# Optimization experiments

Measured on AMD Instinct MI355X. Metric: run time of the kernel, lower is better.

Reference implementation:

```python
import jax, jax.numpy as jnp
import numpy as np

HEAD_NUM = 8
NEG_BIG = 1.0e9


def setup_inputs() -> dict:
    key = jax.random.key(0)
    ks = jax.random.split(key, 9)
    B, S, D = 8, 1024, 512
    return {
        "query": jax.random.normal(ks[0], (B, S, D), dtype=jnp.float32),
        "key": jax.random.normal(ks[1], (B, S, D), dtype=jnp.float32),
        "value": jax.random.normal(ks[2], (B, S, D), dtype=jnp.float32),
        "query_mask": jax.random.randint(ks[3], (B, S), 0, 2, dtype=jnp.int32),
        "key_mask": jax.random.randint(ks[4], (B, S), 0, 2, dtype=jnp.int32),
        "Wq": jax.random.normal(ks[5], (D, D), dtype=jnp.float32) * (1.0 / np.sqrt(D)),
        "Wk": jax.random.normal(ks[6], (D, D), dtype=jnp.float32) * (1.0 / np.sqrt(D)),
        "Wv": jax.random.normal(ks[7], (D, D), dtype=jnp.float32) * (1.0 / np.sqrt(D)),
        "Wo": jax.random.normal(ks[8], (D, D), dtype=jnp.float32) * (1.0 / np.sqrt(D)),
    }


def _split_heads(x, h):
    # TF: tf.concat(tf.split(x, h, axis=2), axis=0) -> (h*B, S, D//h), head-major rows
    return jnp.concatenate(jnp.split(x, h, axis=2), axis=0)


def reference(query, key, value, query_mask, key_mask, Wq, Wk, Wv, Wo):
    H = HEAD_NUM
    B, Sq, Dq = query.shape
    Sk = key.shape[1]
    D = value.shape[-1]

    q = query @ Wq   # (B, Sq, D)
    k = key @ Wk     # (B, Sk, D)
    v = value @ Wv   # (B, Sk, D)

    q_ = _split_heads(q, H)  # (H*B, Sq, D/H)
    k_ = _split_heads(k, H)
    v_ = _split_heads(v, H)

    # TF _reshape_mask: tile then reshape -> batch-major (b*H + h) rows (faithful)
    km = jnp.reshape(jnp.tile(key_mask[:, None, :], (1, H, 1)), (-1, Sk))

    sims = jnp.einsum('bqd,bkd->bqk', q_, k_) / jnp.sqrt(jnp.float32(Dq))

    # causal band mask (sequence_mask=True)
    ones = jnp.ones((Sq, Sk), dtype=jnp.float32)
    causal = ones - jnp.tril(ones)
    sims = sims - causal[None, :, :] * NEG_BIG

    # additive key padding mask
    sims = sims - (1.0 - km[:, None, :].astype(jnp.float32)) * NEG_BIG

    att = jax.nn.softmax(sims, axis=-1)            # (H*B, Sq, Sk)
    out = jnp.einsum('bqk,bkd->bqd', att, v_)      # (H*B, Sq, D/H)

    # faithful TF recombination: reshape (-1, H, Sq, D/H) -> transpose -> (-1, Sq, D)
    out = out.reshape(-1, H, Sq, D // H).transpose(0, 2, 1, 3).reshape(-1, Sq, D)

    out = out @ Wo
    out = jax.nn.relu(out)
    out = out * query_mask[:, :, None].astype(jnp.float32)
    return out
```

## Files before the change

### kernel.cpp

```cpp
#include <hip/hip_runtime.h>
#include <hip/hip_bf16.h>

typedef __bf16 bf16_t;
typedef __bf16 bf16x8 __attribute__((ext_vector_type(8)));
typedef float f32x4 __attribute__((ext_vector_type(4)));

static __device__ __forceinline__ f32x4 mfma16x16x32(bf16x8 a, bf16x8 b, f32x4 c) {
    return __builtin_amdgcn_mfma_f32_16x16x32_bf16(a, b, c, 0, 0, 0);
}

__global__ __launch_bounds__(256, 2) void gemm_qkv(
        const float* __restrict__ Aq, const float* __restrict__ Ak, const float* __restrict__ Av,
        const float* __restrict__ Wq, const float* __restrict__ Wk, const float* __restrict__ Wv,
        bf16_t* __restrict__ Oq, bf16_t* __restrict__ Ok, bf16_t* __restrict__ Ov) {
    __shared__ bf16_t As[128][40];
    __shared__ bf16_t Bs[128][40];

    const int tid  = threadIdx.x;
    const int lane = tid & 63;
    const int wave = tid >> 6;
    const int l15  = lane & 15;
    const int kgrp = lane >> 4;
    const int wr   = wave >> 1;
    const int wc   = wave & 1;

    const int row0 = blockIdx.x * 128;
    const int col0 = blockIdx.y * 128;
    const int z    = blockIdx.z;

    const float* A = (z == 0) ? Aq : (z == 1) ? Ak : Av;
    const float* W = (z == 0) ? Wq : (z == 1) ? Wk : Wv;

    const int ar  = tid >> 1;
    const int ach = (tid & 1) * 16;
    const int bc  = tid & 127;
    const int bkh = (tid >> 7) * 16;

    f32x4 acc[4][4];
    #pragma unroll
    for (int m = 0; m < 4; ++m)
        #pragma unroll
        for (int n = 0; n < 4; ++n) acc[m][n] = (f32x4){0.f, 0.f, 0.f, 0.f};

    float4 areg[4];
    float  breg[16];
    const float* Abase = A + (size_t)(row0 + ar) * 512 + ach;
    const float* Wbase = W + (size_t)bkh * 512 + col0 + bc;

    #pragma unroll
    for (int i = 0; i < 4; ++i) areg[i] = *(const float4*)(Abase + i * 4);
    #pragma unroll
    for (int i = 0; i < 16; ++i) breg[i] = Wbase[(size_t)i * 512];

    for (int kb0 = 0; kb0 < 512; kb0 += 32) {
        __syncthreads();
        {
            bf16x8 w0, w1;
            #pragma unroll
            for (int i = 0; i < 4; ++i) { w0[i] = (bf16_t)(&areg[0].x)[i]; w0[i + 4] = (bf16_t)(&areg[1].x)[i]; }
            #pragma unroll
            for (int i = 0; i < 4; ++i) { w1[i] = (bf16_t)(&areg[2].x)[i]; w1[i + 4] = (bf16_t)(&areg[3].x)[i]; }
            *(bf16x8*)&As[ar][ach]     = w0;
            *(bf16x8*)&As[ar][ach + 8] = w1;
            bf16x8 b0, b1;
            #pragma unroll
            for (int i = 0; i < 8; ++i) { b0[i] = (bf16_t)breg[i]; b1[i] = (bf16_t)breg[i + 8]; }
            *(bf16x8*)&Bs[bc][bkh]     = b0;
            *(bf16x8*)&Bs[bc][bkh + 8] = b1;
        }
        __syncthreads();
        if (kb0 + 32 < 512) {
            const float* An = Abase + kb0 + 32;
            #pragma unroll
            for (int i = 0; i < 4; ++i) areg[i] = *(const float4*)(An + i * 4);
            const float* Wn = Wbase + (size_t)(kb0 + 32) * 512;
            #pragma unroll
            for (int i = 0; i < 16; ++i) breg[i] = Wn[(size_t)i * 512];
        }
        bf16x8 af[4], bf[4];
        #pragma unroll
        for (int m = 0; m < 4; ++m) af[m] = *(const bf16x8*)&As[wr * 64 + m * 16 + l15][kgrp * 8];
        #pragma unroll
        for (int n = 0; n < 4; ++n) bf[n] = *(const bf16x8*)&Bs[wc * 64 + n * 16 + l15][kgrp * 8];
        __builtin_amdgcn_s_setprio(1);
        #pragma unroll
        for (int m = 0; m < 4; ++m)
            #pragma unroll
            for (int n = 0; n < 4; ++n)
                acc[m][n] = mfma16x16x32(af[m], bf[n], acc[m][n]);
        __builtin_amdgcn_s_setprio(0);
    }

    bf16_t* O = (z == 0) ? Oq : (z == 1) ? Ok : Ov;
    #pragma unroll
    for (int m = 0; m < 4; ++m)
        #pragma unroll
        for (int j = 0; j < 4; ++j) {
            const int r = row0 + wr * 64 + m * 16 + kgrp * 4 + j;
            #pragma unroll
            for (int n = 0; n < 4; ++n) {
                const int c = col0 + wc * 64 + n * 16 + l15;
                if (z < 2) {
                    O[(size_t)r * 512 + c] = (bf16_t)acc[m][n][j];
                } else {
                    const int bb = r >> 10, ss = r & 1023;
                    O[((size_t)bb * 512 + c) * 1024 + ss] = (bf16_t)acc[m][n][j];
                }
            }
        }
}

__global__ __launch_bounds__(256, 2) void gemm_out(const bf16_t* __restrict__ Ab,
                                                   const float* __restrict__ W,
                                                   float* __restrict__ Out,
                                                   const int* __restrict__ qmask) {
    __shared__ bf16_t As[128][40];
    __shared__ bf16_t Bs[128][40];

    const int tid  = threadIdx.x;
    const int lane = tid & 63;
    const int wave = tid >> 6;
    const int l15  = lane & 15;
    const int kgrp = lane >> 4;
    const int wr   = wave >> 1;
    const int wc   = wave & 1;

    const int row0 = blockIdx.x * 128;
    const int col0 = blockIdx.y * 128;

    const int ar  = tid >> 1;
    const int ach = (tid & 1) * 16;
    const int bc  = tid & 127;
    const int bkh = (tid >> 7) * 16;

    f32x4 acc[4][4];
    #pragma unroll
    for (int m = 0; m < 4; ++m)
        #pragma unroll
        for (int n = 0; n < 4; ++n) acc[m][n] = (f32x4){0.f, 0.f, 0.f, 0.f};

    bf16x8 areg[2];
    float  breg[16];
    const bf16_t* Abase = Ab + (size_t)(row0 + ar) * 512 + ach;
    const float*  Wbase = W + (size_t)bkh * 512 + col0 + bc;

    areg[0] = *(const bf16x8*)Abase;
    areg[1] = *(const bf16x8*)(Abase + 8);
    #pragma unroll
    for (int i = 0; i < 16; ++i) breg[i] = Wbase[(size_t)i * 512];

    for (int kb0 = 0; kb0 < 512; kb0 += 32) {
        __syncthreads();
        *(bf16x8*)&As[ar][ach]     = areg[0];
        *(bf16x8*)&As[ar][ach + 8] = areg[1];
        {
            bf16x8 b0, b1;
            #pragma unroll
            for (int i = 0; i < 8; ++i) { b0[i] = (bf16_t)breg[i]; b1[i] = (bf16_t)breg[i + 8]; }
            *(bf16x8*)&Bs[bc][bkh]     = b0;
            *(bf16x8*)&Bs[bc][bkh + 8] = b1;
        }
        __syncthreads();
        if (kb0 + 32 < 512) {
            const bf16_t* An = Abase + kb0 + 32;
            areg[0] = *(const bf16x8*)An;
            areg[1] = *(const bf16x8*)(An + 8);
            const float* Wn = Wbase + (size_t)(kb0 + 32) * 512;
            #pragma unroll
            for (int i = 0; i < 16; ++i) breg[i] = Wn[(size_t)i * 512];
        }
        bf16x8 af[4], bf[4];
        #pragma unroll
        for (int m = 0; m < 4; ++m) af[m] = *(const bf16x8*)&As[wr * 64 + m * 16 + l15][kgrp * 8];
        #pragma unroll
        for (int n = 0; n < 4; ++n) bf[n] = *(const bf16x8*)&Bs[wc * 64 + n * 16 + l15][kgrp * 8];
        __builtin_amdgcn_s_setprio(1);
        #pragma unroll
        for (int m = 0; m < 4; ++m)
            #pragma unroll
            for (int n = 0; n < 4; ++n)
                acc[m][n] = mfma16x16x32(af[m], bf[n], acc[m][n]);
        __builtin_amdgcn_s_setprio(0);
    }

    #pragma unroll
    for (int m = 0; m < 4; ++m)
        #pragma unroll
        for (int j = 0; j < 4; ++j) {
            const int r = row0 + wr * 64 + m * 16 + kgrp * 4 + j;
            const float fq = (float)qmask[r];
            #pragma unroll
            for (int n = 0; n < 4; ++n) {
                const int c = col0 + wc * 64 + n * 16 + l15;
                Out[(size_t)r * 512 + c] = fmaxf(acc[m][n][j], 0.0f) * fq;
            }
        }
}

__global__ __launch_bounds__(256, 3) void attn_flash(const bf16_t* __restrict__ qb,
                                                     const bf16_t* __restrict__ kb,
                                                     const bf16_t* __restrict__ vtb,
                                                     const int* __restrict__ key_mask,
                                                     bf16_t* __restrict__ attout) {
    __shared__ char shbuf[34816];
    bf16_t (*P)[32][68] = (bf16_t(*)[32][68])shbuf;
    float (*Omg)[32][66] = (float(*)[32][66])shbuf;
    float* mmg = (float*)(shbuf + 33792);
    float* lmg = (float*)(shbuf + 33792 + 512);

    const int tid  = threadIdx.x;
    const int lane = tid & 63;
    const int w    = tid >> 6;
    const int l15  = lane & 15;
    const int kgrp = lane >> 4;

    const int hb = blockIdx.x;
    const int h  = hb >> 3;
    const int b  = hb & 7;
    const int qw = (31 - (int)blockIdx.y) * 32;

    const size_t bS512 = (size_t)b * 1024 * 512;
    const int hoff = h * 64;
    const int* km = key_mask + h * 1024;

    int kmv = km[lane];
    unsigned long long bal = __ballot(kmv != 0);
    int first1 = bal ? (__ffsll(bal) - 1) : 64;
    const int ntiles = (qw < first1) ? 16 : ((qw + 95) >> 6);

    bf16x8 aq[2][2];
    #pragma unroll
    for (int rf = 0; rf < 2; ++rf)
        #pragma unroll
        for (int ks = 0; ks < 2; ++ks)
            aq[rf][ks] = *(const bf16x8*)(qb + bS512 + (size_t)(qw + rf * 16 + l15) * 512
                                          + hoff + ks * 32 + kgrp * 8);

    f32x4 O[2][4];
    float m[2][4], l[2][4];
    #pragma unroll
    for (int rf = 0; rf < 2; ++rf) {
        #pragma unroll
        for (int df = 0; df < 4; ++df) O[rf][df] = (f32x4){0.f, 0.f, 0.f, 0.f};
        #pragma unroll
        for (int j = 0; j < 4; ++j) { m[rf][j] = -3.0e38f; l[rf][j] = 0.f; }
    }

    const float scale = 0.044194173824159216f;
    const bf16_t* kbase = kb + bS512 + hoff;
    const bf16_t* vbase = vtb + ((size_t)b * 512 + hoff) * 1024;

    for (int kt = w; kt < ntiles; kt += 4) {
        const int kt0 = kt * 64;

        f32x4 S[2][4];
        #pragma unroll
        for (int rf = 0; rf < 2; ++rf)
            #pragma unroll
            for (int cf = 0; cf < 4; ++cf) S[rf][cf] = (f32x4){0.f, 0.f, 0.f, 0.f};

        __builtin_amdgcn_s_setprio(1);
        #pragma unroll
        for (int cf = 0; cf < 4; ++cf) {
            const bf16_t* krow = kbase + (size_t)(kt0 + cf * 16 + l15) * 512 + kgrp * 8;
            bf16x8 bk0 = *(const bf16x8*)krow;
            bf16x8 bk1 = *(const bf16x8*)(krow + 32);
            S[0][cf] = mfma16x16x32(aq[0][0], bk0, S[0][cf]);
            S[0][cf] = mfma16x16x32(aq[0][1], bk1, S[0][cf]);
            S[1][cf] = mfma16x16x32(aq[1][0], bk0, S[1][cf]);
            S[1][cf] = mfma16x16x32(aq[1][1], bk1, S[1][cf]);
        }
        __builtin_amdgcn_s_setprio(0);

        float kmadd[4];
        #pragma unroll
        for (int cf = 0; cf < 4; ++cf)
            kmadd[cf] = (km[kt0 + cf * 16 + l15] == 0) ? 1.0e9f : 0.0f;

        float mx[2][4];
        #pragma unroll
        for (int rf = 0; rf < 2; ++rf)
            #pragma unroll
            for (int j = 0; j < 4; ++j) {
                const int qrow = qw + rf * 16 + kgrp * 4 + j;
                float mj = -3.0e38f;
                #pragma unroll
                for (int cf = 0; cf < 4; ++cf) {
                    float s = S[rf][cf][j] * scale;
                    if (kt0 + cf * 16 + l15 > qrow) s -= 1.0e9f;
                    s -= kmadd[cf];
                    S[rf][cf][j] = s;
                    mj = fmaxf(mj, s);
                }
                mx[rf][j] = mj;
            }
        #pragma unroll
        for (int off = 1; off < 16; off <<= 1)
            #pragma unroll
            for (int rf = 0; rf < 2; ++rf)
                #pragma unroll
                for (int j = 0; j < 4; ++j)
                    mx[rf][j] = fmaxf(mx[rf][j], __shfl_xor(mx[rf][j], off));

        float fac[2][4];
        #pragma unroll
        for (int rf = 0; rf < 2; ++rf)
            #pragma unroll
            for (int j = 0; j < 4; ++j) {
                float mn = fmaxf(m[rf][j], mx[rf][j]);
                fac[rf][j] = __expf(m[rf][j] - mn);
                m[rf][j] = mn;
            }
        #pragma unroll
        for (int rf = 0; rf < 2; ++rf)
            #pragma unroll
            for (int j = 0; j < 4; ++j) {
                float ps = 0.f;
                #pragma unroll
                for (int cf = 0; cf < 4; ++cf) {
                    float p = __expf(S[rf][cf][j] - m[rf][j]);
                    S[rf][cf][j] = p;
                    ps += p;
                }
                l[rf][j] = l[rf][j] * fac[rf][j] + ps;
            }
        #pragma unroll
        for (int rf = 0; rf < 2; ++rf)
            #pragma unroll
            for (int df = 0; df < 4; ++df)
                #pragma unroll
                for (int j = 0; j < 4; ++j)
                    O[rf][df][j] *= fac[rf][j];

        #pragma unroll
        for (int rf = 0; rf < 2; ++rf)
            #pragma unroll
            for (int cf = 0; cf < 4; ++cf)
                #pragma unroll
                for (int j = 0; j < 4; ++j)
                    P[w][rf * 16 + kgrp * 4 + j][cf * 16 + l15] = (bf16_t)S[rf][cf][j];
        asm volatile("s_waitcnt lgkmcnt(0)" ::: "memory");

        bf16x8 pa[2][2];
        #pragma unroll
        for (int rf = 0; rf < 2; ++rf)
            #pragma unroll
            for (int ks = 0; ks < 2; ++ks)
                pa[rf][ks] = *(const bf16x8*)&P[w][rf * 16 + l15][ks * 32 + kgrp * 8];

        __builtin_amdgcn_s_setprio(1);
        #pragma unroll
        for (int df = 0; df < 4; ++df) {
            const bf16_t* vrow = vbase + (size_t)(df * 16 + l15) * 1024 + kt0 + kgrp * 8;
            bf16x8 vf0 = *(const bf16x8*)vrow;
            bf16x8 vf1 = *(const bf16x8*)(vrow + 32);
            O[0][df] = mfma16x16x32(pa[0][0], vf0, O[0][df]);
            O[0][df] = mfma16x16x32(pa[0][1], vf1, O[0][df]);
            O[1][df] = mfma16x16x32(pa[1][0], vf0, O[1][df]);
            O[1][df] = mfma16x16x32(pa[1][1], vf1, O[1][df]);
        }
        __builtin_amdgcn_s_setprio(0);
    }

    __syncthreads();

    #pragma unroll
    for (int rf = 0; rf < 2; ++rf)
        #pragma unroll
        for (int j = 0; j < 4; ++j) {
            float lv = l[rf][j];
            #pragma unroll
            for (int off = 1; off < 16; off <<= 1) lv += __shfl_xor(lv, off);
            l[rf][j] = lv;
        }

    #pragma unroll
    for (int rf = 0; rf < 2; ++rf)
        #pragma unroll
        for (int df = 0; df < 4; ++df)
            #pragma unroll
            for (int j = 0; j < 4; ++j)
                Omg[w][rf * 16 + kgrp * 4 + j][df * 16 + l15] = O[rf][df][j];
    if (l15 == 0) {
        #pragma unroll
        for (int rf = 0; rf < 2; ++rf)
            #pragma unroll
            for (int j = 0; j < 4; ++j) {
                mmg[w * 32 + rf * 16 + kgrp * 4 + j] = m[rf][j];
                lmg[w * 32 + rf * 16 + kgrp * 4 + j] = l[rf][j];
            }
    }
    __syncthreads();

    {
        const int r  = tid >> 3;
        const int c0 = (tid & 7) * 8;
        float m0 = mmg[r], m1 = mmg[32 + r], m2 = mmg[64 + r], m3 = mmg[96 + r];
        float M = fmaxf(fmaxf(m0, m1), fmaxf(m2, m3));
        float f0 = __expf(m0 - M), f1 = __expf(m1 - M);
        float f2 = __expf(m2 - M), f3 = __expf(m3 - M);
        float ls = lmg[r] * f0 + lmg[32 + r] * f1 + lmg[64 + r] * f2 + lmg[96 + r] * f3;
        float inv = 1.0f / ls;
        bf16_t outv[8];
        #pragma unroll
        for (int i = 0; i < 8; ++i) {
            float acc = Omg[0][r][c0 + i] * f0 + Omg[1][r][c0 + i] * f1
                      + Omg[2][r][c0 + i] * f2 + Omg[3][r][c0 + i] * f3;
            outv[i] = (bf16_t)(acc * inv);
        }
        *(bf16x8*)&attout[(size_t)(h * 1024 + qw + r) * 512 + b * 64 + c0] = *(bf16x8*)outv;
    }
}

extern "C" void kernel_launch(void* const* d_in, const int* in_sizes, int n_in,
                              void* d_out, int out_size, void* d_ws, size_t ws_size,
                              hipStream_t stream) {
    const float* query = (const float*)d_in[0];
    const float* key   = (const float*)d_in[1];
    const float* value = (const float*)d_in[2];
    const int*   qmask = (const int*)d_in[3];
    const int*   kmask = (const int*)d_in[4];
    const float* Wq    = (const float*)d_in[5];
    const float* Wk    = (const float*)d_in[6];
    const float* Wv    = (const float*)d_in[7];
    const float* Wo    = (const float*)d_in[8];
    float* out = (float*)d_out;

    const size_t NELEM = (size_t)8 * 1024 * 512;
    bf16_t* qb  = (bf16_t*)d_ws;
    bf16_t* kb  = qb + NELEM;
    bf16_t* vtb = kb + NELEM;
    bf16_t* ab  = vtb + NELEM;

    gemm_qkv<<<dim3(64, 4, 3), dim3(256), 0, stream>>>(query, key, value, Wq, Wk, Wv, qb, kb, vtb);
    attn_flash<<<dim3(64, 32), dim3(256), 0, stream>>>(qb, kb, vtb, kmask, ab);
    gemm_out<<<dim3(64, 4), dim3(256), 0, stream>>>(ab, Wo, out, qmask);
}
```

Measured before the change: 110.0 us.

## Pair mirrored causal query chunks per block and fold softmax scale into Q

Each attention block now handles two query chunks, y and 31-y, so causal work per block is balanced. This halves the grid, and tiles from the two chunks are interleaved in proportion. The softmax scale and log2(e) are folded into the Q projection epilogue, so the kernel can use exp2 directly and skip the per-score multiply. The causal comparison is also skipped for tiles wholly below the diagonal. In exchange, register pressure doubles from two sets of accumulators and Q fragments, which may lower occupancy, and there is a second merge phase with extra barriers.

```diff
diff --git a/kernel.cpp b/kernel.cpp
--- a/kernel.cpp
+++ b/kernel.cpp
@@ -4,6 +4,9 @@
 typedef __bf16 bf16_t;
 typedef __bf16 bf16x8 __attribute__((ext_vector_type(8)));
 typedef float f32x4 __attribute__((ext_vector_type(4)));
+
+#define CPOW 1.4426950409e9f
+#define QSCALE 0.063758715f
 
 static __device__ __forceinline__ f32x4 mfma16x16x32(bf16x8 a, bf16x8 b, f32x4 c) {
     return __builtin_amdgcn_mfma_f32_16x16x32_bf16(a, b, c, 0, 0, 0);
@@ -92,6 +95,7 @@
     }
 
     bf16_t* O = (z == 0) ? Oq : (z == 1) ? Ok : Ov;
+    const float esc = (z == 0) ? QSCALE : 1.0f;
     #pragma unroll
     for (int m = 0; m < 4; ++m)
         #pragma unroll
@@ -101,7 +105,7 @@
             for (int n = 0; n < 4; ++n) {
                 const int c = col0 + wc * 64 + n * 16 + l15;
                 if (z < 2) {
-                    O[(size_t)r * 512 + c] = (bf16_t)acc[m][n][j];
+                    O[(size_t)r * 512 + c] = (bf16_t)(acc[m][n][j] * esc);
                 } else {
                     const int bb = r >> 10, ss = r & 1023;
                     O[((size_t)bb * 512 + c) * 1024 + ss] = (bf16_t)acc[m][n][j];
@@ -217,7 +221,9 @@
     const int hb = blockIdx.x;
     const int h  = hb >> 3;
     const int b  = hb & 7;
-    const int qw = (31 - (int)blockIdx.y) * 32;
+    const int y  = blockIdx.y;
+    const int qwA = y * 32;
+    const int qwB = (31 - y) * 32;
 
     const size_t bS512 = (size_t)b * 1024 * 512;
     const int hoff = h * 64;
@@ -226,31 +232,37 @@
     int kmv = km[lane];
     unsigned long long bal = __ballot(kmv != 0);
     int first1 = bal ? (__ffsll(bal) - 1) : 64;
-    const int ntiles = (qw < first1) ? 16 : ((qw + 95) >> 6);
-
-    bf16x8 aq[2][2];
+    const int ntA = (qwA < first1) ? 16 : ((qwA + 95) >> 6);
+    const int ntB = (qwB < first1) ? 16 : ((qwB + 95) >> 6);
+    const int na  = (ntA > w) ? ((ntA - w + 3) >> 2) : 0;
+    const int nb  = (ntB > w) ? ((ntB - w + 3) >> 2) : 0;
+
+    bf16x8 aqA[2][2], aqB[2][2];
     #pragma unroll
     for (int rf = 0; rf < 2; ++rf)
         #pragma unroll
-        for (int ks = 0; ks < 2; ++ks)
-            aq[rf][ks] = *(const bf16x8*)(qb + bS512 + (size_t)(qw + rf * 16 + l15) * 512
-                                          + hoff + ks * 32 + kgrp * 8);
-
-    f32x4 O[2][4];
-    float m[2][4], l[2][4];
+        for (int ks = 0; ks < 2; ++ks) {
+            aqA[rf][ks] = *(const bf16x8*)(qb + bS512 + (size_t)(qwA + rf * 16 + l15) * 512
+                                           + hoff + ks * 32 + kgrp * 8);
+            aqB[rf][ks] = *(const bf16x8*)(qb + bS512 + (size_t)(qwB + rf * 16 + l15) * 512
+                                           + hoff + ks * 32 + kgrp * 8);
+        }
+
+    f32x4 OA[2][4], OB[2][4];
+    float mA[2][4], lA[2][4], mB[2][4], lB[2][4];
     #pragma unroll
     for (int rf = 0; rf < 2; ++rf) {
         #pragma unroll
-        for (int df = 0; df < 4; ++df) O[rf][df] = (f32x4){0.f, 0.f, 0.f, 0.f};
-        #pragma unroll
-        for (int j = 0; j < 4; ++j) { m[rf][j] = -3.0e38f; l[rf][j] = 0.f; }
+        for (int df = 0; df < 4; ++df) { OA[rf][df] = (f32x4){0.f,0.f,0.f,0.f}; OB[rf][df] = (f32x4){0.f,0.f,0.f,0.f}; }
+        #pragma unroll
+        for (int j = 0; j < 4; ++j) { mA[rf][j] = -3.0e38f; lA[rf][j] = 0.f; mB[rf][j] = -3.0e38f; lB[rf][j] = 0.f; }
     }
 
-    const float scale = 0.044194173824159216f;
     const bf16_t* kbase = kb + bS512 + hoff;
     const bf16_t* vbase = vtb + ((size_t)b * 512 + hoff) * 1024;
 
-    for (int kt = w; kt < ntiles; kt += 4) {
+    auto processTile = [&](int kt, int qwX, bf16x8 (&aq)[2][2], f32x4 (&O)[2][4],
+                           float (&m)[2][4], float (&l)[2][4], int pslot) {
         const int kt0 = kt * 64;
 
         f32x4 S[2][4];
@@ -275,20 +287,21 @@
         float kmadd[4];
         #pragma unroll
         for (int cf = 0; cf < 4; ++cf)
-            kmadd[cf] = (km[kt0 + cf * 16 + l15] == 0) ? 1.0e9f : 0.0f;
-
+            kmadd[cf] = (km[kt0 + cf * 16 + l15] == 0) ? CPOW : 0.0f;
+
+        const bool needC = (kt0 + 63 > qwX);
         float mx[2][4];
         #pragma unroll
         for (int rf = 0; rf < 2; ++rf)
             #pragma unroll
             for (int j = 0; j < 4; ++j) {
-                const int qrow = qw + rf * 16 + kgrp * 4 + j;
+                const int qrow = qwX + rf * 16 + kgrp * 4 + j;
                 float mj = -3.0e38f;
                 #pragma unroll
                 for (int cf = 0; cf < 4; ++cf) {
-                    float s = S[rf][cf][j] * scale;
-                    if (kt0 + cf * 16 + l15 > qrow) s -= 1.0e9f;
-                    s -= kmadd[cf];
+                    float sub = kmadd[cf];
+                    if (needC && (kt0 + cf * 16 + l15 > qrow)) sub += CPOW;
+                    float s = S[rf][cf][j] - sub;
                     S[rf][cf][j] = s;
                     mj = fmaxf(mj, s);
                 }
@@ -308,7 +321,7 @@
             #pragma unroll
             for (int j = 0; j < 4; ++j) {
                 float mn = fmaxf(m[rf][j], mx[rf][j]);
-                fac[rf][j] = __expf(m[rf][j] - mn);
+                fac[rf][j] = __builtin_amdgcn_exp2f(m[rf][j] - mn);
                 m[rf][j] = mn;
             }
         #pragma unroll
@@ -318,7 +331,7 @@
                 float ps = 0.f;
                 #pragma unroll
                 for (int cf = 0; cf < 4; ++cf) {
-                    float p = __expf(S[rf][cf][j] - m[rf][j]);
+                    float p = __builtin_amdgcn_exp2f(S[rf][cf][j] - m[rf][j]);
                     S[rf][cf][j] = p;
                     ps += p;
                 }
@@ -338,7 +351,7 @@
             for (int cf = 0; cf < 4; ++cf)
                 #pragma unroll
                 for (int j = 0; j < 4; ++j)
-                    P[w][rf * 16 + kgrp * 4 + j][cf * 16 + l15] = (bf16_t)S[rf][cf][j];
+                    P[pslot][rf * 16 + kgrp * 4 + j][cf * 16 + l15] = (bf16_t)S[rf][cf][j];
         asm volatile("s_waitcnt lgkmcnt(0)" ::: "memory");
 
         bf16x8 pa[2][2];
@@ -346,7 +359,7 @@
         for (int rf = 0; rf < 2; ++rf)
             #pragma unroll
             for (int ks = 0; ks < 2; ++ks)
-                pa[rf][ks] = *(const bf16x8*)&P[w][rf * 16 + l15][ks * 32 + kgrp * 8];
+                pa[rf][ks] = *(const bf16x8*)&P[pslot][rf * 16 + l15][ks * 32 + kgrp * 8];
 
         __builtin_amdgcn_s_setprio(1);
         #pragma unroll
@@ -360,56 +373,72 @@
             O[1][df] = mfma16x16x32(pa[1][1], vf1, O[1][df]);
         }
         __builtin_amdgcn_s_setprio(0);
+    };
+
+    {
+        int ia = 0, ib = 0;
+        const int total = na + nb;
+        for (int it = 0; it < total; ++it) {
+            bool doA;
+            if (ia >= na) doA = false;
+            else if (ib >= nb) doA = true;
+            else doA = (ia * nb <= ib * na);
+            if (doA) { processTile(w + 4 * ia, qwA, aqA, OA, mA, lA, w);     ++ia; }
+            else     { processTile(w + 4 * ib, qwB, aqB, OB, mB, lB, 4 + w); ++ib; }
+        }
     }
 
+    auto mergeChunk = [&](int qwX, f32x4 (&O)[2][4], float (&m)[2][4], float (&l)[2][4]) {
+        #pragma unroll
+        for (int rf = 0; rf < 2; ++rf)
+            #pragma unroll
+            for (int j = 0; j < 4; ++j) {
+                float lv = l[rf][j];
+                #pragma unroll
+                for (int off = 1; off < 16; off <<= 1) lv += __shfl_xor(lv, off);
+                l[rf][j] = lv;
+            }
+        #pragma unroll
+        for (int rf = 0; rf < 2; ++rf)
+            #pragma unroll
+            for (int df = 0; df < 4; ++df)
+                #pragma unroll
+                for (int j = 0; j < 4; ++j)
+                    Omg[w][rf * 16 + kgrp * 4 + j][df * 16 + l15] = O[rf][df][j];
+        if (l15 == 0) {
+            #pragma unroll
+            for (int rf = 0; rf < 2; ++rf)
+                #pragma unroll
+                for (int j = 0; j < 4; ++j) {
+                    mmg[w * 32 + rf * 16 + kgrp * 4 + j] = m[rf][j];
+                    lmg[w * 32 + rf * 16 + kgrp * 4 + j] = l[rf][j];
+                }
+        }
+        __syncthreads();
+        {
+            const int r  = tid >> 3;
+            const int c0 = (tid & 7) * 8;
+            float m0 = mmg[r], m1 = mmg[32 + r], m2 = mmg[64 + r], m3 = mmg[96 + r];
+            float M = fmaxf(fmaxf(m0, m1), fmaxf(m2, m3));
+            float f0 = __builtin_amdgcn_exp2f(m0 - M), f1 = __builtin_amdgcn_exp2f(m1 - M);
+            float f2 = __builtin_amdgcn_exp2f(m2 - M), f3 = __builtin_amdgcn_exp2f(m3 - M);
+            float ls = lmg[r] * f0 + lmg[32 + r] * f1 + lmg[64 + r] * f2 + lmg[96 + r] * f3;
+            float inv = 1.0f / ls;
+            bf16_t outv[8];
+            #pragma unroll
+            for (int i = 0; i < 8; ++i) {
+                float acc = Omg[0][r][c0 + i] * f0 + Omg[1][r][c0 + i] * f1
+                          + Omg[2][r][c0 + i] * f2 + Omg[3][r][c0 + i] * f3;
+                outv[i] = (bf16_t)(acc * inv);
+            }
+            *(bf16x8*)&attout[(size_t)(h * 1024 + qwX + r) * 512 + b * 64 + c0] = *(bf16x8*)outv;
+        }
+    };
+
     __syncthreads();
-
-    #pragma unroll
-    for (int rf = 0; rf < 2; ++rf)
-        #pragma unroll
-        for (int j = 0; j < 4; ++j) {
-            float lv = l[rf][j];
-            #pragma unroll
-            for (int off = 1; off < 16; off <<= 1) lv += __shfl_xor(lv, off);
-            l[rf][j] = lv;
-        }
-
-    #pragma unroll
-    for (int rf = 0; rf < 2; ++rf)
-        #pragma unroll
-        for (int df = 0; df < 4; ++df)
-            #pragma unroll
-            for (int j = 0; j < 4; ++j)
-                Omg[w][rf * 16 + kgrp * 4 + j][df * 16 + l15] = O[rf][df][j];
-    if (l15 == 0) {
-        #pragma unroll
-        for (int rf = 0; rf < 2; ++rf)
-            #pragma unroll
-            for (int j = 0; j < 4; ++j) {
-                mmg[w * 32 + rf * 16 + kgrp * 4 + j] = m[rf][j];
-                lmg[w * 32 + rf * 16 + kgrp * 4 + j] = l[rf][j];
-            }
-    }
+    mergeChunk(qwA, OA, mA, lA);
     __syncthreads();
-
-    {
-        const int r  = tid >> 3;
-        const int c0 = (tid & 7) * 8;
-        float m0 = mmg[r], m1 = mmg[32 + r], m2 = mmg[64 + r], m3 = mmg[96 + r];
-        float M = fmaxf(fmaxf(m0, m1), fmaxf(m2, m3));
-        float f0 = __expf(m0 - M), f1 = __expf(m1 - M);
-        float f2 = __expf(m2 - M), f3 = __expf(m3 - M);
-        float ls = lmg[r] * f0 + lmg[32 + r] * f1 + lmg[64 + r] * f2 + lmg[96 + r] * f3;
-        float inv = 1.0f / ls;
-        bf16_t outv[8];
-        #pragma unroll
-        for (int i = 0; i < 8; ++i) {
-            float acc = Omg[0][r][c0 + i] * f0 + Omg[1][r][c0 + i] * f1
-                      + Omg[2][r][c0 + i] * f2 + Omg[3][r][c0 + i] * f3;
-            outv[i] = (bf16_t)(acc * inv);
-        }
-        *(bf16x8*)&attout[(size_t)(h * 1024 + qw + r) * 512 + b * 64 + c0] = *(bf16x8*)outv;
-    }
+    mergeChunk(qwB, OB, mB, lB);
 }
 
 extern "C" void kernel_launch(void* const* d_in, const int* in_sizes, int n_in,
@@ -433,6 +462,6 @@
     bf16_t* ab  = vtb + NELEM;
 
     gemm_qkv<<<dim3(64, 4, 3), dim3(256), 0, stream>>>(query, key, value, Wq, Wk, Wv, qb, kb, vtb);
-    attn_flash<<<dim3(64, 32), dim3(256), 0, stream>>>(qb, kb, vtb, kmask, ab);
+    attn_flash<<<dim3(64, 16), dim3(256), 0, stream>>>(qb, kb, vtb, kmask, ab);
     gemm_out<<<dim3(64, 4), dim3(256), 0, stream>>>(ab, Wo, out, qmask);
 }
```

After: 170.8 us. +55.2%, slower.

## Fold softmax scale and log2e into Q projection, use exp2, shrink attention LDS

Applied to the files above, without the earlier changes.

Pre-scales Q in the projection GEMM epilogue by scale*log2(e), so the attention kernel can drop the per-element multiply and use the hardware exp2 instruction with mask constants scaled to match. The causal-mask comparison is skipped for key tiles entirely below the diagonal. The cross-wave merge buffer is stored in bf16 instead of fp32, which shrinks shared memory so the launch bound can be raised from 3 to 6 blocks per CU. In exchange, the partial outputs lose precision before they are merged, and register pressure is tighter at the higher occupancy target.

```diff
diff --git a/kernel.cpp b/kernel.cpp
--- a/kernel.cpp
+++ b/kernel.cpp
@@ -4,6 +4,9 @@
 typedef __bf16 bf16_t;
 typedef __bf16 bf16x8 __attribute__((ext_vector_type(8)));
 typedef float f32x4 __attribute__((ext_vector_type(4)));
+
+#define CPOW 1.4426950409e9f
+#define QSCALE 0.063758715f
 
 static __device__ __forceinline__ f32x4 mfma16x16x32(bf16x8 a, bf16x8 b, f32x4 c) {
     return __builtin_amdgcn_mfma_f32_16x16x32_bf16(a, b, c, 0, 0, 0);
@@ -92,6 +95,7 @@
     }
 
     bf16_t* O = (z == 0) ? Oq : (z == 1) ? Ok : Ov;
+    const float esc = (z == 0) ? QSCALE : 1.0f;
     #pragma unroll
     for (int m = 0; m < 4; ++m)
         #pragma unroll
@@ -101,7 +105,7 @@
             for (int n = 0; n < 4; ++n) {
                 const int c = col0 + wc * 64 + n * 16 + l15;
                 if (z < 2) {
-                    O[(size_t)r * 512 + c] = (bf16_t)acc[m][n][j];
+                    O[(size_t)r * 512 + c] = (bf16_t)(acc[m][n][j] * esc);
                 } else {
                     const int bb = r >> 10, ss = r & 1023;
                     O[((size_t)bb * 512 + c) * 1024 + ss] = (bf16_t)acc[m][n][j];
@@ -197,16 +201,16 @@
         }
 }
 
-__global__ __launch_bounds__(256, 3) void attn_flash(const bf16_t* __restrict__ qb,
+__global__ __launch_bounds__(256, 6) void attn_flash(const bf16_t* __restrict__ qb,
                                                      const bf16_t* __restrict__ kb,
                                                      const bf16_t* __restrict__ vtb,
                                                      const int* __restrict__ key_mask,
                                                      bf16_t* __restrict__ attout) {
-    __shared__ char shbuf[34816];
-    bf16_t (*P)[32][68] = (bf16_t(*)[32][68])shbuf;
-    float (*Omg)[32][66] = (float(*)[32][66])shbuf;
-    float* mmg = (float*)(shbuf + 33792);
-    float* lmg = (float*)(shbuf + 33792 + 512);
+    __shared__ char shbuf[19456];
+    bf16_t (*P)[32][72]   = (bf16_t(*)[32][72])shbuf;
+    bf16_t (*Omg)[32][72] = (bf16_t(*)[32][72])shbuf;
+    float* mmg = (float*)(shbuf + 18432);
+    float* lmg = (float*)(shbuf + 18432 + 512);
 
     const int tid  = threadIdx.x;
     const int lane = tid & 63;
@@ -246,7 +250,6 @@
         for (int j = 0; j < 4; ++j) { m[rf][j] = -3.0e38f; l[rf][j] = 0.f; }
     }
 
-    const float scale = 0.044194173824159216f;
     const bf16_t* kbase = kb + bS512 + hoff;
     const bf16_t* vbase = vtb + ((size_t)b * 512 + hoff) * 1024;
 
@@ -275,8 +278,9 @@
         float kmadd[4];
         #pragma unroll
         for (int cf = 0; cf < 4; ++cf)
-            kmadd[cf] = (km[kt0 + cf * 16 + l15] == 0) ? 1.0e9f : 0.0f;
-
+            kmadd[cf] = (km[kt0 + cf * 16 + l15] == 0) ? CPOW : 0.0f;
+
+        const bool needC = (kt0 + 63 > qw);
         float mx[2][4];
         #pragma unroll
         for (int rf = 0; rf < 2; ++rf)
@@ -286,9 +290,9 @@
                 float mj = -3.0e38f;
                 #pragma unroll
                 for (int cf = 0; cf < 4; ++cf) {
-                    float s = S[rf][cf][j] * scale;
-                    if (kt0 + cf * 16 + l15 > qrow) s -= 1.0e9f;
-                    s -= kmadd[cf];
+                    float sub = kmadd[cf];
+                    if (needC && (kt0 + cf * 16 + l15 > qrow)) sub += CPOW;
+                    float s = S[rf][cf][j] - sub;
                     S[rf][cf][j] = s;
                     mj = fmaxf(mj, s);
                 }
@@ -308,7 +312,7 @@
             #pragma unroll
             for (int j = 0; j < 4; ++j) {
                 float mn = fmaxf(m[rf][j], mx[rf][j]);
-                fac[rf][j] = __expf(m[rf][j] - mn);
+                fac[rf][j] = __builtin_amdgcn_exp2f(m[rf][j] - mn);
                 m[rf][j] = mn;
             }
         #pragma unroll
@@ -318,7 +322,7 @@
                 float ps = 0.f;
                 #pragma unroll
                 for (int cf = 0; cf < 4; ++cf) {
-                    float p = __expf(S[rf][cf][j] - m[rf][j]);
+                    float p = __builtin_amdgcn_exp2f(S[rf][cf][j] - m[rf][j]);
                     S[rf][cf][j] = p;
                     ps += p;
                 }
@@ -380,7 +384,7 @@
         for (int df = 0; df < 4; ++df)
             #pragma unroll
             for (int j = 0; j < 4; ++j)
-                Omg[w][rf * 16 + kgrp * 4 + j][df * 16 + l15] = O[rf][df][j];
+                Omg[w][rf * 16 + kgrp * 4 + j][df * 16 + l15] = (bf16_t)O[rf][df][j];
     if (l15 == 0) {
         #pragma unroll
         for (int rf = 0; rf < 2; ++rf)
@@ -397,15 +401,19 @@
         const int c0 = (tid & 7) * 8;
         float m0 = mmg[r], m1 = mmg[32 + r], m2 = mmg[64 + r], m3 = mmg[96 + r];
         float M = fmaxf(fmaxf(m0, m1), fmaxf(m2, m3));
-        float f0 = __expf(m0 - M), f1 = __expf(m1 - M);
-        float f2 = __expf(m2 - M), f3 = __expf(m3 - M);
+        float f0 = __builtin_amdgcn_exp2f(m0 - M), f1 = __builtin_amdgcn_exp2f(m1 - M);
+        float f2 = __builtin_amdgcn_exp2f(m2 - M), f3 = __builtin_amdgcn_exp2f(m3 - M);
         float ls = lmg[r] * f0 + lmg[32 + r] * f1 + lmg[64 + r] * f2 + lmg[96 + r] * f3;
         float inv = 1.0f / ls;
+        bf16x8 o0 = *(const bf16x8*)&Omg[0][r][c0];
+        bf16x8 o1 = *(const bf16x8*)&Omg[1][r][c0];
+        bf16x8 o2 = *(const bf16x8*)&Omg[2][r][c0];
+        bf16x8 o3 = *(const bf16x8*)&Omg[3][r][c0];
         bf16_t outv[8];
         #pragma unroll
         for (int i = 0; i < 8; ++i) {
-            float acc = Omg[0][r][c0 + i] * f0 + Omg[1][r][c0 + i] * f1
-                      + Omg[2][r][c0 + i] * f2 + Omg[3][r][c0 + i] * f3;
+            float acc = (float)o0[i] * f0 + (float)o1[i] * f1
+                      + (float)o2[i] * f2 + (float)o3[i] * f3;
             outv[i] = (bf16_t)(acc * inv);
         }
         *(bf16x8*)&attout[(size_t)(h * 1024 + qw + r) * 512 + b * 64 + c0] = *(bf16x8*)outv;
```

Result: slower. 221.4 us (+101.2%).
